# Kernel tuning notes

Hardware: AMD Instinct MI355X
Metric: run time of the kernel (lower is better)

Reference implementation:

```python
import jax, jax.numpy as jnp
import numpy as np

N_HEADS = 16
EMBED = 1024
HEAD_SIZE = 64
BLOCK = 2048
BATCH = 4


def setup_inputs() -> dict:
    key = jax.random.key(0)
    ks = jax.random.split(key, 6)
    s = 1.0 / np.sqrt(EMBED)
    X = jax.random.normal(ks[0], (BATCH, BLOCK, EMBED), dtype=jnp.float32)
    Wq = jax.random.normal(ks[1], (N_HEADS, EMBED, HEAD_SIZE), dtype=jnp.float32) * s
    Wk = jax.random.normal(ks[2], (N_HEADS, EMBED, HEAD_SIZE), dtype=jnp.float32) * s
    Wv = jax.random.normal(ks[3], (N_HEADS, EMBED, HEAD_SIZE), dtype=jnp.float32) * s
    Wo = jax.random.normal(ks[4], (EMBED, EMBED), dtype=jnp.float32) * s
    bo = jnp.zeros((EMBED,), dtype=jnp.float32)
    return {"X": X, "Wq": Wq, "Wk": Wk, "Wv": Wv, "Wo": Wo, "bo": bo}


def reference(X, Wq, Wk, Wv, Wo, bo):
    # X: [B, S, E]; Wq/Wk/Wv: [H, E, Dh]
    q = jnp.einsum("bse,hed->bhsd", X, Wq)
    k = jnp.einsum("bse,hed->bhsd", X, Wk)
    v = jnp.einsum("bse,hed->bhsd", X, Wv)
    scale = 1.0 / np.sqrt(HEAD_SIZE)
    scores = jnp.einsum("bhsd,bhtd->bhst", q, k) * scale  # [B,H,S,S]
    S = X.shape[1]
    causal = jnp.tril(jnp.ones((S, S), dtype=bool))
    scores = jnp.where(causal, scores, -jnp.inf)
    wei = jax.nn.softmax(scores, axis=-1)
    # dropout p=0.2 treated as identity (eval mode) for deterministic reference
    out = jnp.einsum("bhst,bhtd->bhsd", wei, v)  # [B,H,S,Dh]
    out = out.transpose(0, 2, 1, 3).reshape(X.shape[0], S, N_HEADS * HEAD_SIZE)
    return out @ Wo.T + bo
```

## Files before the change

### kernel.cpp

```cpp
#include <hip/hip_runtime.h>
#include <stdint.h>


typedef __bf16 bf16_t;
typedef __bf16 bf16x4 __attribute__((ext_vector_type(4)));
typedef __bf16 bf16x8 __attribute__((ext_vector_type(8)));
typedef float  f32x4  __attribute__((ext_vector_type(4)));
typedef float  f32x16 __attribute__((ext_vector_type(16)));
typedef unsigned int u32;

union V8 { bf16x8 v8; bf16x4 h[2]; u32 w[4]; };

__device__ __forceinline__ void gload_lds16(const void* g, void* l) {
  __builtin_amdgcn_global_load_lds((const __attribute__((address_space(1))) void*)g,
                                   (__attribute__((address_space(3))) void*)l, 16, 0, 0);
}


__global__ void mha_cvt_bf16(const float* __restrict__ in, bf16_t* __restrict__ out) {
  size_t i = ((size_t)blockIdx.x * 256 + threadIdx.x) * 8;
  const float4* p = (const float4*)(in + i);
  float4 a = p[0], b = p[1];
  bf16x8 o;
  o[0] = (__bf16)a.x; o[1] = (__bf16)a.y; o[2] = (__bf16)a.z; o[3] = (__bf16)a.w;
  o[4] = (__bf16)b.x; o[5] = (__bf16)b.y; o[6] = (__bf16)b.z; o[7] = (__bf16)b.w;
  *(bf16x8*)(out + i) = o;
}

__global__ void mha_prep_w(const float* __restrict__ Wq, const float* __restrict__ Wk,
                           const float* __restrict__ Wv, bf16_t* __restrict__ Wt) {
  __shared__ float tile[64][65];
  const int e0 = blockIdx.x * 64;
  const int mh = blockIdx.y;
  const int mat = mh >> 4, h = mh & 15;
  const float* W = (mat == 0) ? Wq : (mat == 1) ? Wk : Wv;
  #pragma unroll
  for (int i = 0; i < 16; i++) {
    int idx = threadIdx.x + i * 256;
    int er = idx >> 6, d = idx & 63;
    tile[er][d] = W[(size_t)(h * 1024 + e0 + er) * 64 + d];
  }
  __syncthreads();
  #pragma unroll
  for (int i = 0; i < 16; i++) {
    int idx = threadIdx.x + i * 256;
    int dr = idx >> 6, ec = idx & 63;
    Wt[(size_t)(mat * 1024 + h * 64 + dr) * 1024 + e0 + ec] = (bf16_t)tile[ec][dr];
  }
}


template <int MODE>
__global__ __launch_bounds__(256) void gemm_bt(const bf16_t* __restrict__ A,
                                               const bf16_t* __restrict__ Bt,
                                               void* __restrict__ Cout,
                                               const float* __restrict__ bias,
                                               int M, int N, int K) {
  __shared__ bf16_t lA[128 * 32];
  __shared__ bf16_t lB[128 * 32];
  const int tid = threadIdx.x;
  const int l = tid & 63, w = tid >> 6;
  const int g = l >> 4, lg = l & 15;
  const int wr = w >> 1, wc = w & 1;
  const long brow = (long)blockIdx.y * 128;
  const long bcol = (long)blockIdx.x * 128;

  f32x4 acc[4][4];
  #pragma unroll
  for (int m = 0; m < 4; m++)
    #pragma unroll
    for (int n = 0; n < 4; n++) acc[m][n] = (f32x4){0.f, 0.f, 0.f, 0.f};

  const bf16_t* Ab = A + brow * K;
  const bf16_t* Bb = Bt + bcol * K;
  const int c0 = tid, c1 = tid + 256;
  const int r0 = c0 >> 2, o0 = (c0 & 3) * 8;
  const int r1 = c1 >> 2, o1 = (c1 & 3) * 8;

  for (int k0 = 0; k0 < K; k0 += 32) {
    __syncthreads();
    gload_lds16(Ab + (long)r0 * K + k0 + o0, lA + c0 * 8);
    gload_lds16(Ab + (long)r1 * K + k0 + o1, lA + c1 * 8);
    gload_lds16(Bb + (long)r0 * K + k0 + o0, lB + c0 * 8);
    gload_lds16(Bb + (long)r1 * K + k0 + o1, lB + c1 * 8);
    __syncthreads();
    bf16x8 af[4], bfr[4];
    #pragma unroll
    for (int m = 0; m < 4; m++)
      af[m] = *(const bf16x8*)(lA + (wr * 64 + m * 16 + lg) * 32 + g * 8);
    #pragma unroll
    for (int n = 0; n < 4; n++)
      bfr[n] = *(const bf16x8*)(lB + (wc * 64 + n * 16 + lg) * 32 + g * 8);
    #pragma unroll
    for (int m = 0; m < 4; m++)
      #pragma unroll
      for (int n = 0; n < 4; n++)
        acc[m][n] = __builtin_amdgcn_mfma_f32_16x16x32_bf16(af[m], bfr[n], acc[m][n], 0, 0, 0);
  }

  #pragma unroll
  for (int m = 0; m < 4; m++) {
    #pragma unroll
    for (int n = 0; n < 4; n++) {
      long row0 = brow + wr * 64 + m * 16 + g * 4;
      long col  = bcol + wc * 64 + n * 16 + lg;
      if (MODE == 0) {
        bf16_t* C = (bf16_t*)Cout;
        #pragma unroll
        for (int r = 0; r < 4; r++) C[(row0 + r) * N + col] = (bf16_t)acc[m][n][r];
      } else {
        float* C = (float*)Cout;
        float bv = bias[col];
        #pragma unroll
        for (int r = 0; r < 4; r++) C[(row0 + r) * N + col] = acc[m][n][r] + bv;
      }
    }
  }
}


__global__ __launch_bounds__(256, 4) void mha_attn3(const bf16_t* __restrict__ QKV,
                                                    bf16_t* __restrict__ AO) {
  __shared__ __align__(16) char smem[32768];
  const int tid = threadIdx.x;
  const int l = tid & 63, w = tid >> 6;
  const int q31 = l & 31;
  const int hi = l >> 5;
  const int hb = (l >> 4) & 1;
  const int lg = l & 15;

  const int bid = blockIdx.x;
  const int xcd = bid & 7, ii = bid >> 3;
  const int bh = xcd * 8 + (ii & 7);
  const int stripe = 15 - (ii >> 3);
  const int b = bh >> 4, h = bh & 15;

  const int qw = stripe * 128 + w * 32;
  const bf16_t* Qp = QKV + (size_t)b * 2048 * 3072 + h * 64;
  const bf16_t* Kp = Qp + 1024;
  const bf16_t* Vp = Qp + 2048;

  bf16x8 qf[4];
  {
    const bf16_t* qrow = Qp + (size_t)(qw + q31) * 3072 + hi * 8;
    #pragma unroll
    for (int ks = 0; ks < 4; ks++) qf[ks] = *(const bf16x8*)(qrow + ks * 16);
  }

  f32x16 o0, o1;
  #pragma unroll
  for (int r = 0; r < 16; r++) { o0[r] = 0.f; o1[r] = 0.f; }
  float m = -1e30f, lsum = 0.f;
  const float Cf = 0.18033688011112042f;

  const int tmaxw = 2 * stripe + 1 + (w >> 1);
  const int T = 2 * stripe + 2;
  const u32 ldsbase = (u32)(uintptr_t)(__attribute__((address_space(3))) char*)smem;

  auto stage = [&](int tt, int bi) {
    char* kb = smem + bi * 8192;
    char* vb = smem + 16384 + bi * 8192;
    #pragma unroll
    for (int it = 0; it < 2; it++) {
      int c = tid + it * 256;
      int row = c >> 3, cb = (c & 7) * 16;
      int scb = cb ^ ((row & 7) << 4);
      gload_lds16(Kp + (size_t)(tt * 64 + row) * 3072 + (scb >> 1), kb + c * 16);
      int st = c >> 5, qq = c & 31;
      int j = (st >> 2) * 16 + (qq >> 1), d = (st & 3) * 16 + (qq & 1) * 8;
      gload_lds16(Vp + (size_t)(tt * 64 + j) * 3072 + d, vb + c * 16);
    }
  };

  stage(0, 0);
  for (int t = 0; t < T; t++) {
    const int cur = t & 1;
    if (t + 1 < T) {
      stage(t + 1, cur ^ 1);
      __builtin_amdgcn_sched_barrier(0);
      asm volatile("s_waitcnt vmcnt(4)" ::: "memory");
    } else {
      __builtin_amdgcn_sched_barrier(0);
      asm volatile("s_waitcnt vmcnt(0)" ::: "memory");
    }
    __builtin_amdgcn_sched_barrier(0);
    __builtin_amdgcn_s_barrier();
    __builtin_amdgcn_sched_barrier(0);

    const bool active = (t < tmaxw);
    u32 paw[4][4];
    if (active) {
      f32x16 p0, p1;
      #pragma unroll
      for (int r = 0; r < 16; r++) { p0[r] = 0.f; p1[r] = 0.f; }
      {
        const char* kb = smem + cur * 8192;
        const int rb0 = q31 * 128;
        const int swz = (l & 7) << 4;
        __builtin_amdgcn_s_setprio(1);
        #pragma unroll
        for (int ks = 0; ks < 4; ks++) {
          int colb = ((ks << 5) | (hi << 4)) ^ swz;
          bf16x8 kf0 = *(const bf16x8*)(kb + rb0 + colb);
          bf16x8 kf1 = *(const bf16x8*)(kb + 4096 + rb0 + colb);
          p0 = __builtin_amdgcn_mfma_f32_32x32x16_bf16(kf0, qf[ks], p0, 0, 0, 0);
          p1 = __builtin_amdgcn_mfma_f32_32x32x16_bf16(kf1, qf[ks], p1, 0, 0, 0);
        }
        __builtin_amdgcn_s_setprio(0);
      }
      if (t == tmaxw - 1) {
        int q = qw + q31;
        int kvb = t * 64 + 4 * hi;
        #pragma unroll
        for (int r = 0; r < 16; r++) {
          int kv0 = kvb + (r & 3) + 8 * (r >> 2);
          if (kv0 > q) p0[r] = -1e30f;
          if (kv0 + 32 > q) p1[r] = -1e30f;
        }
      }
      float t8[8];
      #pragma unroll
      for (int r = 0; r < 8; r++)
        t8[r] = fmaxf(fmaxf(p0[r], p0[r + 8]), fmaxf(p1[r], p1[r + 8]));
      float pm = fmaxf(fmaxf(fmaxf(t8[0], t8[4]), fmaxf(t8[1], t8[5])),
                       fmaxf(fmaxf(t8[2], t8[6]), fmaxf(t8[3], t8[7])));
      pm = fmaxf(pm, __shfl_xor(pm, 32));
      if (!__all(pm - m <= 64.f)) {
        float mn = fmaxf(m, pm);
        float alpha = exp2f((m - mn) * Cf);
        #pragma unroll
        for (int r = 0; r < 16; r++) { o0[r] *= alpha; o1[r] *= alpha; }
        lsum *= alpha;
        m = mn;
      }
      float mc = m * Cf;
      #pragma unroll
      for (int r = 0; r < 16; r++) p0[r] = exp2f(fmaf(p0[r], Cf, -mc));
      #pragma unroll
      for (int r = 0; r < 16; r++) p1[r] = exp2f(fmaf(p1[r], Cf, -mc));
      float s8[8];
      #pragma unroll
      for (int r = 0; r < 8; r++)
        s8[r] = (p0[r] + p0[r + 8]) + (p1[r] + p1[r + 8]);
      float rs = ((s8[0] + s8[1]) + (s8[2] + s8[3])) + ((s8[4] + s8[5]) + (s8[6] + s8[7]));
      rs += __shfl_xor(rs, 32);
      lsum += rs;
      #pragma unroll
      for (int gblk = 0; gblk < 4; gblk++) {
        int base = (gblk & 1) * 8;
        float e0 = (gblk < 2) ? p0[base + 0] : p1[base + 0];
        float e1 = (gblk < 2) ? p0[base + 1] : p1[base + 1];
        float e2 = (gblk < 2) ? p0[base + 2] : p1[base + 2];
        float e3 = (gblk < 2) ? p0[base + 3] : p1[base + 3];
        float e4 = (gblk < 2) ? p0[base + 4] : p1[base + 4];
        float e5 = (gblk < 2) ? p0[base + 5] : p1[base + 5];
        float e6 = (gblk < 2) ? p0[base + 6] : p1[base + 6];
        float e7 = (gblk < 2) ? p0[base + 7] : p1[base + 7];
        u32 u0, u1, v0, v1;
        asm("v_cvt_pk_bf16_f32 %0, %1, %2" : "=v"(u0) : "v"(e0), "v"(e1));
        asm("v_cvt_pk_bf16_f32 %0, %1, %2" : "=v"(u1) : "v"(e2), "v"(e3));
        asm("v_cvt_pk_bf16_f32 %0, %1, %2" : "=v"(v0) : "v"(e4), "v"(e5));
        asm("v_cvt_pk_bf16_f32 %0, %1, %2" : "=v"(v1) : "v"(e6), "v"(e7));
        asm("v_permlane32_swap_b32 %0, %1" : "+v"(u0), "+v"(v0));
        asm("v_permlane32_swap_b32 %0, %1" : "+v"(u1), "+v"(v1));
        paw[gblk][0] = u0; paw[gblk][1] = u1; paw[gblk][2] = v0; paw[gblk][3] = v1;
      }
      V8 vf[2][4];
      u32 vb = ldsbase + 16384u + (u32)cur * 8192u;
      #pragma unroll
      for (int mb = 0; mb < 2; mb++)
        #pragma unroll
        for (int ks = 0; ks < 4; ks++) {
          u32 base = vb + (u32)(((ks * 4 + 2 * mb + hb) << 9) + hi * 256 + lg * 8);
          bf16x4 t0, t1;
          asm volatile("ds_read_b64_tr_b16 %0, %1" : "=v"(t0) : "v"(base));
          asm volatile("ds_read_b64_tr_b16 %0, %1 offset:128" : "=v"(t1) : "v"(base));
          vf[mb][ks].h[0] = t0; vf[mb][ks].h[1] = t1;
        }
      asm volatile("s_waitcnt lgkmcnt(0)" ::: "memory");
      __builtin_amdgcn_sched_barrier(0);
      __builtin_amdgcn_s_setprio(1);
      #pragma unroll
      for (int ks = 0; ks < 4; ks++) {
        V8 pa; pa.w[0] = paw[ks][0]; pa.w[1] = paw[ks][1]; pa.w[2] = paw[ks][2]; pa.w[3] = paw[ks][3];
        o0 = __builtin_amdgcn_mfma_f32_32x32x16_bf16(vf[0][ks].v8, pa.v8, o0, 0, 0, 0);
        o1 = __builtin_amdgcn_mfma_f32_32x32x16_bf16(vf[1][ks].v8, pa.v8, o1, 0, 0, 0);
      }
      __builtin_amdgcn_s_setprio(0);
    }
    __builtin_amdgcn_sched_barrier(0);
    __builtin_amdgcn_s_barrier();
    __builtin_amdgcn_sched_barrier(0);
  }

  float linv = 1.f / lsum;
  __syncthreads();
  bf16_t* ow = (bf16_t*)smem + w * 2048;
  #pragma unroll
  for (int mb = 0; mb < 2; mb++)
    #pragma unroll
    for (int r = 0; r < 16; r += 2) {
      int d = mb * 32 + (r & 3) + 8 * (r >> 2) + 4 * hi;
      float a0 = (mb ? o1[r] : o0[r]) * linv;
      float a1 = (mb ? o1[r + 1] : o0[r + 1]) * linv;
      u32 pk;
      asm("v_cvt_pk_bf16_f32 %0, %1, %2" : "=v"(pk) : "v"(a0), "v"(a1));
      int byteoff = q31 * 128 + ((d * 2) ^ ((q31 & 7) << 4));
      *(u32*)((char*)ow + byteoff) = pk;
    }
  __syncthreads();
  const size_t aorow0 = (size_t)b * 2048 + qw;
  #pragma unroll
  for (int it = 0; it < 4; it++) {
    int idx = it * 64 + l;
    int q = idx >> 3, c = idx & 7;
    bf16x8 v8 = *(const bf16x8*)((const char*)ow + q * 128 + ((c * 16) ^ ((q & 7) << 4)));
    *(bf16x8*)(AO + (aorow0 + q) * 1024 + h * 64 + c * 8) = v8;
  }
}


extern "C" void kernel_launch(void* const* d_in, const int* in_sizes, int n_in,
                              void* d_out, int out_size, void* d_ws, size_t ws_size,
                              hipStream_t stream) {
  (void)in_sizes; (void)n_in; (void)out_size; (void)ws_size;
  const float* X  = (const float*)d_in[0];
  const float* Wq = (const float*)d_in[1];
  const float* Wk = (const float*)d_in[2];
  const float* Wv = (const float*)d_in[3];
  const float* Wo = (const float*)d_in[4];
  const float* bo = (const float*)d_in[5];
  float* out = (float*)d_out;

  char* ws = (char*)d_ws;
  bf16_t* Xb  = (bf16_t*)ws;
  bf16_t* AO  = Xb;
  bf16_t* Wt  = (bf16_t*)(ws + (16u << 20));
  bf16_t* Wob = (bf16_t*)(ws + (22u << 20));
  bf16_t* QKV = (bf16_t*)(ws + (24u << 20));

  mha_cvt_bf16<<<dim3(4096), dim3(256), 0, stream>>>(X, Xb);
  mha_prep_w<<<dim3(16, 48), dim3(256), 0, stream>>>(Wq, Wk, Wv, Wt);
  mha_cvt_bf16<<<dim3(512), dim3(256), 0, stream>>>(Wo, Wob);
  gemm_bt<0><<<dim3(3072 / 128, 8192 / 128), dim3(256), 0, stream>>>(
      Xb, Wt, (void*)QKV, nullptr, 8192, 3072, 1024);
  mha_attn3<<<dim3(1024), dim3(256), 0, stream>>>(QKV, AO);
  gemm_bt<1><<<dim3(1024 / 128, 8192 / 128), dim3(256), 0, stream>>>(
      AO, Wob, (void*)out, bo, 8192, 1024, 1024);
}
```

Measured before the change: 188.5 us.

## Pair long and short causal stripes per workgroup for balanced attention work

Each attention workgroup now handles two query stripes, a high one (15-pair) and a low one (pair), so every workgroup does the same total number of KV tiles and the causal load imbalance goes away. The grid is halved to 512 workgroups, and the K/V prefetch pipeline carries across from the first stripe into the second. The first stripe's accumulators stay in registers until both epilogues run, which raises register pressure, so launch bounds drop to 2 waves per SIMD. Fewer workgroups means less parallelism to hide latency.

```diff
diff --git a/kernel.cpp b/kernel.cpp
--- a/kernel.cpp
+++ b/kernel.cpp
@@ -119,7 +119,7 @@
 }
 
 
-__global__ __launch_bounds__(256, 4) void mha_attn3(const bf16_t* __restrict__ QKV,
+__global__ __launch_bounds__(256, 2) void mha_attn4(const bf16_t* __restrict__ QKV,
                                                     bf16_t* __restrict__ AO) {
   __shared__ __align__(16) char smem[32768];
   const int tid = threadIdx.x;
@@ -130,34 +130,31 @@
   const int lg = l & 15;
 
   const int bid = blockIdx.x;
-  const int xcd = bid & 7, ii = bid >> 3;
-  const int bh = xcd * 8 + (ii & 7);
-  const int stripe = 15 - (ii >> 3);
+  const int wgid = (bid & 7) * 64 + (bid >> 3);
+  const int bh = wgid >> 3, pair = wgid & 7;
   const int b = bh >> 4, h = bh & 15;
-
-  const int qw = stripe * 128 + w * 32;
+  const int s_hi = 15 - pair, s_lo = pair;
+  const int T_hi = 2 * s_hi + 2;
+
   const bf16_t* Qp = QKV + (size_t)b * 2048 * 3072 + h * 64;
   const bf16_t* Kp = Qp + 1024;
   const bf16_t* Vp = Qp + 2048;
 
-  bf16x8 qf[4];
+  bf16x8 qfh[4], qfl[4];
   {
-    const bf16_t* qrow = Qp + (size_t)(qw + q31) * 3072 + hi * 8;
-    #pragma unroll
-    for (int ks = 0; ks < 4; ks++) qf[ks] = *(const bf16x8*)(qrow + ks * 16);
-  }
-
-  f32x16 o0, o1;
-  #pragma unroll
-  for (int r = 0; r < 16; r++) { o0[r] = 0.f; o1[r] = 0.f; }
-  float m = -1e30f, lsum = 0.f;
+    const bf16_t* qr0 = Qp + (size_t)(s_hi * 128 + w * 32 + q31) * 3072 + hi * 8;
+    const bf16_t* qr1 = Qp + (size_t)(s_lo * 128 + w * 32 + q31) * 3072 + hi * 8;
+    #pragma unroll
+    for (int ks = 0; ks < 4; ks++) {
+      qfh[ks] = *(const bf16x8*)(qr0 + ks * 16);
+      qfl[ks] = *(const bf16x8*)(qr1 + ks * 16);
+    }
+  }
+
   const float Cf = 0.18033688011112042f;
-
-  const int tmaxw = 2 * stripe + 1 + (w >> 1);
-  const int T = 2 * stripe + 2;
   const u32 ldsbase = (u32)(uintptr_t)(__attribute__((address_space(3))) char*)smem;
 
-  auto stage = [&](int tt, int bi) {
+  auto stage = [&](int kt, int bi) {
     char* kb = smem + bi * 8192;
     char* vb = smem + 16384 + bi * 8192;
     #pragma unroll
@@ -165,157 +162,184 @@
       int c = tid + it * 256;
       int row = c >> 3, cb = (c & 7) * 16;
       int scb = cb ^ ((row & 7) << 4);
-      gload_lds16(Kp + (size_t)(tt * 64 + row) * 3072 + (scb >> 1), kb + c * 16);
+      gload_lds16(Kp + (size_t)(kt * 64 + row) * 3072 + (scb >> 1), kb + c * 16);
       int st = c >> 5, qq = c & 31;
       int j = (st >> 2) * 16 + (qq >> 1), d = (st & 3) * 16 + (qq & 1) * 8;
-      gload_lds16(Vp + (size_t)(tt * 64 + j) * 3072 + d, vb + c * 16);
+      gload_lds16(Vp + (size_t)(kt * 64 + j) * 3072 + d, vb + c * 16);
     }
   };
 
+  auto epilogue = [&](const f32x16& e0, const f32x16& e1, float ls, int qw) {
+    float linv = 1.f / ls;
+    __syncthreads();
+    bf16_t* ow = (bf16_t*)smem + w * 2048;
+    #pragma unroll
+    for (int mb = 0; mb < 2; mb++)
+      #pragma unroll
+      for (int r = 0; r < 16; r += 2) {
+        int d = mb * 32 + (r & 3) + 8 * (r >> 2) + 4 * hi;
+        float a0 = (mb ? e1[r] : e0[r]) * linv;
+        float a1 = (mb ? e1[r + 1] : e0[r + 1]) * linv;
+        u32 pk;
+        asm("v_cvt_pk_bf16_f32 %0, %1, %2" : "=v"(pk) : "v"(a0), "v"(a1));
+        int byteoff = q31 * 128 + ((d * 2) ^ ((q31 & 7) << 4));
+        *(u32*)((char*)ow + byteoff) = pk;
+      }
+    __syncthreads();
+    const size_t aorow0 = (size_t)b * 2048 + qw;
+    #pragma unroll
+    for (int it = 0; it < 4; it++) {
+      int idx = it * 64 + l;
+      int q = idx >> 3, c = idx & 7;
+      bf16x8 v8 = *(const bf16x8*)((const char*)ow + q * 128 + ((c * 16) ^ ((q & 7) << 4)));
+      *(bf16x8*)(AO + (aorow0 + q) * 1024 + h * 64 + c * 8) = v8;
+    }
+  };
+
+  f32x16 oh0, oh1;
+  float lsum_h = 0.f;
+
   stage(0, 0);
-  for (int t = 0; t < T; t++) {
-    const int cur = t & 1;
-    if (t + 1 < T) {
-      stage(t + 1, cur ^ 1);
+  #pragma unroll
+  for (int st = 0; st < 2; st++) {
+    const int s = st == 0 ? s_hi : s_lo;
+    const int qw = s * 128 + w * 32;
+    const int T = 2 * s + 2;
+    const int tmaxw = 2 * s + 1 + (w >> 1);
+
+    f32x16 o0, o1;
+    #pragma unroll
+    for (int r = 0; r < 16; r++) { o0[r] = 0.f; o1[r] = 0.f; }
+    float m = -1e30f, lsum = 0.f;
+
+    for (int t = 0; t < T; t++) {
+      const int cur = t & 1;
+      const bool last_global = (st == 1) && (t + 1 == T);
+      if (!last_global) {
+        int nk = (st == 0) ? ((t + 1 < T) ? t + 1 : 0) : t + 1;
+        stage(nk, cur ^ 1);
+        __builtin_amdgcn_sched_barrier(0);
+        asm volatile("s_waitcnt vmcnt(4)" ::: "memory");
+      } else {
+        __builtin_amdgcn_sched_barrier(0);
+        asm volatile("s_waitcnt vmcnt(0)" ::: "memory");
+      }
       __builtin_amdgcn_sched_barrier(0);
-      asm volatile("s_waitcnt vmcnt(4)" ::: "memory");
-    } else {
+      __builtin_amdgcn_s_barrier();
       __builtin_amdgcn_sched_barrier(0);
-      asm volatile("s_waitcnt vmcnt(0)" ::: "memory");
-    }
-    __builtin_amdgcn_sched_barrier(0);
-    __builtin_amdgcn_s_barrier();
-    __builtin_amdgcn_sched_barrier(0);
-
-    const bool active = (t < tmaxw);
-    u32 paw[4][4];
-    if (active) {
-      f32x16 p0, p1;
-      #pragma unroll
-      for (int r = 0; r < 16; r++) { p0[r] = 0.f; p1[r] = 0.f; }
-      {
-        const char* kb = smem + cur * 8192;
-        const int rb0 = q31 * 128;
-        const int swz = (l & 7) << 4;
+
+      const bool active = (t < tmaxw);
+      u32 paw[4][4];
+      if (active) {
+        f32x16 p0, p1;
+        #pragma unroll
+        for (int r = 0; r < 16; r++) { p0[r] = 0.f; p1[r] = 0.f; }
+        {
+          const char* kb = smem + cur * 8192;
+          const int rb0 = q31 * 128;
+          const int swz = (l & 7) << 4;
+          __builtin_amdgcn_s_setprio(1);
+          #pragma unroll
+          for (int ks = 0; ks < 4; ks++) {
+            int colb = ((ks << 5) | (hi << 4)) ^ swz;
+            bf16x8 kf0 = *(const bf16x8*)(kb + rb0 + colb);
+            bf16x8 kf1 = *(const bf16x8*)(kb + 4096 + rb0 + colb);
+            bf16x8 qv = st == 0 ? qfh[ks] : qfl[ks];
+            p0 = __builtin_amdgcn_mfma_f32_32x32x16_bf16(kf0, qv, p0, 0, 0, 0);
+            p1 = __builtin_amdgcn_mfma_f32_32x32x16_bf16(kf1, qv, p1, 0, 0, 0);
+          }
+          __builtin_amdgcn_s_setprio(0);
+        }
+        if (t == tmaxw - 1) {
+          int q = qw + q31;
+          int kvb = t * 64 + 4 * hi;
+          #pragma unroll
+          for (int r = 0; r < 16; r++) {
+            int kv0 = kvb + (r & 3) + 8 * (r >> 2);
+            if (kv0 > q) p0[r] = -1e30f;
+            if (kv0 + 32 > q) p1[r] = -1e30f;
+          }
+        }
+        float t8[8];
+        #pragma unroll
+        for (int r = 0; r < 8; r++)
+          t8[r] = fmaxf(fmaxf(p0[r], p0[r + 8]), fmaxf(p1[r], p1[r + 8]));
+        float pm = fmaxf(fmaxf(fmaxf(t8[0], t8[4]), fmaxf(t8[1], t8[5])),
+                         fmaxf(fmaxf(t8[2], t8[6]), fmaxf(t8[3], t8[7])));
+        pm = fmaxf(pm, __shfl_xor(pm, 32));
+        if (!__all(pm - m <= 64.f)) {
+          float mn = fmaxf(m, pm);
+          float alpha = exp2f((m - mn) * Cf);
+          #pragma unroll
+          for (int r = 0; r < 16; r++) { o0[r] *= alpha; o1[r] *= alpha; }
+          lsum *= alpha;
+          m = mn;
+        }
+        float mc = m * Cf;
+        #pragma unroll
+        for (int r = 0; r < 16; r++) p0[r] = exp2f(fmaf(p0[r], Cf, -mc));
+        #pragma unroll
+        for (int r = 0; r < 16; r++) p1[r] = exp2f(fmaf(p1[r], Cf, -mc));
+        float s8[8];
+        #pragma unroll
+        for (int r = 0; r < 8; r++)
+          s8[r] = (p0[r] + p0[r + 8]) + (p1[r] + p1[r + 8]);
+        float rs = ((s8[0] + s8[1]) + (s8[2] + s8[3])) + ((s8[4] + s8[5]) + (s8[6] + s8[7]));
+        rs += __shfl_xor(rs, 32);
+        lsum += rs;
+        #pragma unroll
+        for (int gblk = 0; gblk < 4; gblk++) {
+          int base = (gblk & 1) * 8;
+          float e0 = (gblk < 2) ? p0[base + 0] : p1[base + 0];
+          float e1 = (gblk < 2) ? p0[base + 1] : p1[base + 1];
+          float e2 = (gblk < 2) ? p0[base + 2] : p1[base + 2];
+          float e3 = (gblk < 2) ? p0[base + 3] : p1[base + 3];
+          float e4 = (gblk < 2) ? p0[base + 4] : p1[base + 4];
+          float e5 = (gblk < 2) ? p0[base + 5] : p1[base + 5];
+          float e6 = (gblk < 2) ? p0[base + 6] : p1[base + 6];
+          float e7 = (gblk < 2) ? p0[base + 7] : p1[base + 7];
+          u32 u0, u1, v0, v1;
+          asm("v_cvt_pk_bf16_f32 %0, %1, %2" : "=v"(u0) : "v"(e0), "v"(e1));
+          asm("v_cvt_pk_bf16_f32 %0, %1, %2" : "=v"(u1) : "v"(e2), "v"(e3));
+          asm("v_cvt_pk_bf16_f32 %0, %1, %2" : "=v"(v0) : "v"(e4), "v"(e5));
+          asm("v_cvt_pk_bf16_f32 %0, %1, %2" : "=v"(v1) : "v"(e6), "v"(e7));
+          asm("v_permlane32_swap_b32 %0, %1" : "+v"(u0), "+v"(v0));
+          asm("v_permlane32_swap_b32 %0, %1" : "+v"(u1), "+v"(v1));
+          paw[gblk][0] = u0; paw[gblk][1] = u1; paw[gblk][2] = v0; paw[gblk][3] = v1;
+        }
+        V8 vf[2][4];
+        u32 vb = ldsbase + 16384u + (u32)cur * 8192u;
+        #pragma unroll
+        for (int mb = 0; mb < 2; mb++)
+          #pragma unroll
+          for (int ks = 0; ks < 4; ks++) {
+            u32 base = vb + (u32)(((ks * 4 + 2 * mb + hb) << 9) + hi * 256 + lg * 8);
+            bf16x4 t0, t1;
+            asm volatile("ds_read_b64_tr_b16 %0, %1" : "=v"(t0) : "v"(base));
+            asm volatile("ds_read_b64_tr_b16 %0, %1 offset:128" : "=v"(t1) : "v"(base));
+            vf[mb][ks].h[0] = t0; vf[mb][ks].h[1] = t1;
+          }
+        asm volatile("s_waitcnt lgkmcnt(0)" ::: "memory");
+        __builtin_amdgcn_sched_barrier(0);
         __builtin_amdgcn_s_setprio(1);
         #pragma unroll
         for (int ks = 0; ks < 4; ks++) {
-          int colb = ((ks << 5) | (hi << 4)) ^ swz;
-          bf16x8 kf0 = *(const bf16x8*)(kb + rb0 + colb);
-          bf16x8 kf1 = *(const bf16x8*)(kb + 4096 + rb0 + colb);
-          p0 = __builtin_amdgcn_mfma_f32_32x32x16_bf16(kf0, qf[ks], p0, 0, 0, 0);
-          p1 = __builtin_amdgcn_mfma_f32_32x32x16_bf16(kf1, qf[ks], p1, 0, 0, 0);
+          V8 pa; pa.w[0] = paw[ks][0]; pa.w[1] = paw[ks][1]; pa.w[2] = paw[ks][2]; pa.w[3] = paw[ks][3];
+          o0 = __builtin_amdgcn_mfma_f32_32x32x16_bf16(vf[0][ks].v8, pa.v8, o0, 0, 0, 0);
+          o1 = __builtin_amdgcn_mfma_f32_32x32x16_bf16(vf[1][ks].v8, pa.v8, o1, 0, 0, 0);
         }
         __builtin_amdgcn_s_setprio(0);
       }
-      if (t == tmaxw - 1) {
-        int q = qw + q31;
-        int kvb = t * 64 + 4 * hi;
-        #pragma unroll
-        for (int r = 0; r < 16; r++) {
-          int kv0 = kvb + (r & 3) + 8 * (r >> 2);
-          if (kv0 > q) p0[r] = -1e30f;
-          if (kv0 + 32 > q) p1[r] = -1e30f;
-        }
-      }
-      float t8[8];
-      #pragma unroll
-      for (int r = 0; r < 8; r++)
-        t8[r] = fmaxf(fmaxf(p0[r], p0[r + 8]), fmaxf(p1[r], p1[r + 8]));
-      float pm = fmaxf(fmaxf(fmaxf(t8[0], t8[4]), fmaxf(t8[1], t8[5])),
-                       fmaxf(fmaxf(t8[2], t8[6]), fmaxf(t8[3], t8[7])));
-      pm = fmaxf(pm, __shfl_xor(pm, 32));
-      if (!__all(pm - m <= 64.f)) {
-        float mn = fmaxf(m, pm);
-        float alpha = exp2f((m - mn) * Cf);
-        #pragma unroll
-        for (int r = 0; r < 16; r++) { o0[r] *= alpha; o1[r] *= alpha; }
-        lsum *= alpha;
-        m = mn;
-      }
-      float mc = m * Cf;
-      #pragma unroll
-      for (int r = 0; r < 16; r++) p0[r] = exp2f(fmaf(p0[r], Cf, -mc));
-      #pragma unroll
-      for (int r = 0; r < 16; r++) p1[r] = exp2f(fmaf(p1[r], Cf, -mc));
-      float s8[8];
-      #pragma unroll
-      for (int r = 0; r < 8; r++)
-        s8[r] = (p0[r] + p0[r + 8]) + (p1[r] + p1[r + 8]);
-      float rs = ((s8[0] + s8[1]) + (s8[2] + s8[3])) + ((s8[4] + s8[5]) + (s8[6] + s8[7]));
-      rs += __shfl_xor(rs, 32);
-      lsum += rs;
-      #pragma unroll
-      for (int gblk = 0; gblk < 4; gblk++) {
-        int base = (gblk & 1) * 8;
-        float e0 = (gblk < 2) ? p0[base + 0] : p1[base + 0];
-        float e1 = (gblk < 2) ? p0[base + 1] : p1[base + 1];
-        float e2 = (gblk < 2) ? p0[base + 2] : p1[base + 2];
-        float e3 = (gblk < 2) ? p0[base + 3] : p1[base + 3];
-        float e4 = (gblk < 2) ? p0[base + 4] : p1[base + 4];
-        float e5 = (gblk < 2) ? p0[base + 5] : p1[base + 5];
-        float e6 = (gblk < 2) ? p0[base + 6] : p1[base + 6];
-        float e7 = (gblk < 2) ? p0[base + 7] : p1[base + 7];
-        u32 u0, u1, v0, v1;
-        asm("v_cvt_pk_bf16_f32 %0, %1, %2" : "=v"(u0) : "v"(e0), "v"(e1));
-        asm("v_cvt_pk_bf16_f32 %0, %1, %2" : "=v"(u1) : "v"(e2), "v"(e3));
-        asm("v_cvt_pk_bf16_f32 %0, %1, %2" : "=v"(v0) : "v"(e4), "v"(e5));
-        asm("v_cvt_pk_bf16_f32 %0, %1, %2" : "=v"(v1) : "v"(e6), "v"(e7));
-        asm("v_permlane32_swap_b32 %0, %1" : "+v"(u0), "+v"(v0));
-        asm("v_permlane32_swap_b32 %0, %1" : "+v"(u1), "+v"(v1));
-        paw[gblk][0] = u0; paw[gblk][1] = u1; paw[gblk][2] = v0; paw[gblk][3] = v1;
-      }
-      V8 vf[2][4];
-      u32 vb = ldsbase + 16384u + (u32)cur * 8192u;
-      #pragma unroll
-      for (int mb = 0; mb < 2; mb++)
-        #pragma unroll
-        for (int ks = 0; ks < 4; ks++) {
-          u32 base = vb + (u32)(((ks * 4 + 2 * mb + hb) << 9) + hi * 256 + lg * 8);
-          bf16x4 t0, t1;
-          asm volatile("ds_read_b64_tr_b16 %0, %1" : "=v"(t0) : "v"(base));
-          asm volatile("ds_read_b64_tr_b16 %0, %1 offset:128" : "=v"(t1) : "v"(base));
-          vf[mb][ks].h[0] = t0; vf[mb][ks].h[1] = t1;
-        }
-      asm volatile("s_waitcnt lgkmcnt(0)" ::: "memory");
       __builtin_amdgcn_sched_barrier(0);
-      __builtin_amdgcn_s_setprio(1);
-      #pragma unroll
-      for (int ks = 0; ks < 4; ks++) {
-        V8 pa; pa.w[0] = paw[ks][0]; pa.w[1] = paw[ks][1]; pa.w[2] = paw[ks][2]; pa.w[3] = paw[ks][3];
-        o0 = __builtin_amdgcn_mfma_f32_32x32x16_bf16(vf[0][ks].v8, pa.v8, o0, 0, 0, 0);
-        o1 = __builtin_amdgcn_mfma_f32_32x32x16_bf16(vf[1][ks].v8, pa.v8, o1, 0, 0, 0);
-      }
-      __builtin_amdgcn_s_setprio(0);
-    }
-    __builtin_amdgcn_sched_barrier(0);
-    __builtin_amdgcn_s_barrier();
-    __builtin_amdgcn_sched_barrier(0);
-  }
-
-  float linv = 1.f / lsum;
-  __syncthreads();
-  bf16_t* ow = (bf16_t*)smem + w * 2048;
-  #pragma unroll
-  for (int mb = 0; mb < 2; mb++)
-    #pragma unroll
-    for (int r = 0; r < 16; r += 2) {
-      int d = mb * 32 + (r & 3) + 8 * (r >> 2) + 4 * hi;
-      float a0 = (mb ? o1[r] : o0[r]) * linv;
-      float a1 = (mb ? o1[r + 1] : o0[r + 1]) * linv;
-      u32 pk;
-      asm("v_cvt_pk_bf16_f32 %0, %1, %2" : "=v"(pk) : "v"(a0), "v"(a1));
-      int byteoff = q31 * 128 + ((d * 2) ^ ((q31 & 7) << 4));
-      *(u32*)((char*)ow + byteoff) = pk;
-    }
-  __syncthreads();
-  const size_t aorow0 = (size_t)b * 2048 + qw;
-  #pragma unroll
-  for (int it = 0; it < 4; it++) {
-    int idx = it * 64 + l;
-    int q = idx >> 3, c = idx & 7;
-    bf16x8 v8 = *(const bf16x8*)((const char*)ow + q * 128 + ((c * 16) ^ ((q & 7) << 4)));
-    *(bf16x8*)(AO + (aorow0 + q) * 1024 + h * 64 + c * 8) = v8;
+      __builtin_amdgcn_s_barrier();
+      __builtin_amdgcn_sched_barrier(0);
+    }
+
+    if (st == 0) { oh0 = o0; oh1 = o1; lsum_h = lsum; }
+    else {
+      epilogue(oh0, oh1, lsum_h, s_hi * 128 + w * 32);
+      epilogue(o0, o1, lsum, qw);
+    }
   }
 }
 
@@ -344,7 +368,7 @@
   mha_cvt_bf16<<<dim3(512), dim3(256), 0, stream>>>(Wo, Wob);
   gemm_bt<0><<<dim3(3072 / 128, 8192 / 128), dim3(256), 0, stream>>>(
       Xb, Wt, (void*)QKV, nullptr, 8192, 3072, 1024);
-  mha_attn3<<<dim3(1024), dim3(256), 0, stream>>>(QKV, AO);
+  mha_attn4<<<dim3(512), dim3(256), 0, stream>>>(QKV, AO);
   gemm_bt<1><<<dim3(1024 / 128, 8192 / 128), dim3(256), 0, stream>>>(
       AO, Wob, (void*)out, bo, 8192, 1024, 1024);
 }
```

Result: slower. 192.9 us (+2.3%).

## Add 256x256 pipelined QKV GEMM and rebalance causal attention block order

Applied to the files above, without the earlier changes.

Replaces the 128x128 QKV projection GEMM with a 512-thread 256x256 tile kernel. It uses 128KB of LDS holding a three-slot ring of K chunks, staged with direct global-to-LDS loads, and spreads the loads across eight compute phases with s_setprio around the MFMA bursts. Block IDs are swizzled across XCDs for reuse. The attention kernel's block-to-stripe mapping is also changed, pairing short and long causal stripes so per-wave work is more even. This trades occupancy (one large block per CU) for more data reuse per block and overlap of loads with compute.

```diff
diff --git a/kernel.cpp b/kernel.cpp
--- a/kernel.cpp
+++ b/kernel.cpp
@@ -47,6 +47,115 @@
     int dr = idx >> 6, ec = idx & 63;
     Wt[(size_t)(mat * 1024 + h * 64 + dr) * 1024 + e0 + ec] = (bf16_t)tile[ec][dr];
   }
+}
+
+
+__global__ __launch_bounds__(512, 2) void gemm256(const bf16_t* __restrict__ A,
+                                                  const bf16_t* __restrict__ Bt,
+                                                  bf16_t* __restrict__ C,
+                                                  int M, int N, int K) {
+  __shared__ __align__(16) char lds[131072];
+  const int tid = threadIdx.x;
+  const int l = tid & 63, w = tid >> 6;
+  const int g = l >> 4, lg = l & 15;
+  const int wr = w >> 2, wc = w & 3;
+  const int bid = blockIdx.x;
+  const int nbn = N >> 8;
+  const int gsw = (bid & 7) * (gridDim.x >> 3) + (bid >> 3);
+  const long brow = (long)(gsw / nbn) * 256;
+  const long bcol = (long)(gsw % nbn) * 256;
+
+  f32x4 acc[8][4];
+  #pragma unroll
+  for (int im = 0; im < 8; im++)
+    #pragma unroll
+    for (int n = 0; n < 4; n++) acc[im][n] = (f32x4){0.f, 0.f, 0.f, 0.f};
+
+  auto stage = [&](const bf16_t* base, long trow, int k0, int region) {
+    #pragma unroll
+    for (int j = 0; j < 2; j++) {
+      int p = (tid + j * 512) * 16;
+      gload_lds16(base + (trow + (p >> 6)) * (long)K + k0 + ((p & 63) >> 1),
+                  lds + region + p);
+    }
+  };
+
+  stage(A,  brow, 0,  0);
+  stage(Bt, bcol, 0,  65536);
+  stage(A,  brow, 32, 16384);
+  stage(Bt, bcol, 32, 65536 + 16384);
+  stage(A,  brow, 64, 32768);
+  stage(Bt, bcol, 64, 65536 + 32768);
+  asm volatile("s_waitcnt vmcnt(4)" ::: "memory");
+  __builtin_amdgcn_s_barrier();
+  __builtin_amdgcn_sched_barrier(0);
+
+  const int nIter = K >> 7;
+  for (int t = 0; t < nIter; t++) {
+    const bool more = (t + 1 < nIter);
+    const int kb = t * 128;
+    #pragma unroll
+    for (int ph = 0; ph < 8; ph++) {
+      const int slot = ph >> 2;
+      const int kh = (ph >> 1) & 1, mq = ph & 1;
+      bf16x8 af[4], bfv[4];
+      {
+        const char* pA = lds + slot * 32768 + kh * 16384;
+        const char* pB = pA + 65536;
+        #pragma unroll
+        for (int m = 0; m < 4; m++) {
+          int wrow = wr * 128 + mq * 64 + m * 16 + lg;
+          af[m] = *(const bf16x8*)(pA + wrow * 64 + g * 16);
+        }
+        #pragma unroll
+        for (int n = 0; n < 4; n++) {
+          int wrow = wc * 64 + n * 16 + lg;
+          bfv[n] = *(const bf16x8*)(pB + wrow * 64 + g * 16);
+        }
+      }
+      if (ph == 0)      stage(A,  brow, kb + 96,  32768 + 16384);
+      else if (ph == 1) stage(Bt, bcol, kb + 96,  65536 + 32768 + 16384);
+      else if (more) {
+        if (ph == 2)      stage(A,  brow, kb + 128, 0);
+        else if (ph == 3) stage(Bt, bcol, kb + 128, 65536);
+        else if (ph == 4) stage(A,  brow, kb + 160, 16384);
+        else if (ph == 5) stage(Bt, bcol, kb + 160, 65536 + 16384);
+        else if (ph == 6) stage(A,  brow, kb + 192, 32768);
+        else              stage(Bt, bcol, kb + 192, 65536 + 32768);
+      }
+      __builtin_amdgcn_s_barrier();
+      asm volatile("s_waitcnt lgkmcnt(0)" ::: "memory");
+      __builtin_amdgcn_sched_barrier(0);
+      __builtin_amdgcn_s_setprio(1);
+      #pragma unroll
+      for (int m = 0; m < 4; m++)
+        #pragma unroll
+        for (int n = 0; n < 4; n++)
+          acc[mq * 4 + m][n] =
+              __builtin_amdgcn_mfma_f32_16x16x32_bf16(af[m], bfv[n], acc[mq * 4 + m][n], 0, 0, 0);
+      __builtin_amdgcn_s_setprio(0);
+      __builtin_amdgcn_sched_barrier(0);
+      if (ph == 3) {
+        if (more) asm volatile("s_waitcnt vmcnt(4)" ::: "memory");
+        else      asm volatile("s_waitcnt vmcnt(0)" ::: "memory");
+      } else if (ph == 7 && more) {
+        asm volatile("s_waitcnt vmcnt(4)" ::: "memory");
+      }
+      __builtin_amdgcn_s_barrier();
+      __builtin_amdgcn_sched_barrier(0);
+    }
+  }
+
+  #pragma unroll
+  for (int im = 0; im < 8; im++)
+    #pragma unroll
+    for (int n = 0; n < 4; n++) {
+      long row0 = brow + wr * 128 + im * 16 + g * 4;
+      long col  = bcol + wc * 64 + n * 16 + lg;
+      #pragma unroll
+      for (int r = 0; r < 4; r++)
+        C[(row0 + r) * N + col] = (bf16_t)acc[im][n][r];
+    }
 }
 
 
@@ -105,14 +214,14 @@
       long row0 = brow + wr * 64 + m * 16 + g * 4;
       long col  = bcol + wc * 64 + n * 16 + lg;
       if (MODE == 0) {
-        bf16_t* C = (bf16_t*)Cout;
-        #pragma unroll
-        for (int r = 0; r < 4; r++) C[(row0 + r) * N + col] = (bf16_t)acc[m][n][r];
+        bf16_t* Cb = (bf16_t*)Cout;
+        #pragma unroll
+        for (int r = 0; r < 4; r++) Cb[(row0 + r) * N + col] = (bf16_t)acc[m][n][r];
       } else {
-        float* C = (float*)Cout;
+        float* Cf = (float*)Cout;
         float bv = bias[col];
         #pragma unroll
-        for (int r = 0; r < 4; r++) C[(row0 + r) * N + col] = acc[m][n][r] + bv;
+        for (int r = 0; r < 4; r++) Cf[(row0 + r) * N + col] = acc[m][n][r] + bv;
       }
     }
   }
@@ -130,9 +239,10 @@
   const int lg = l & 15;
 
   const int bid = blockIdx.x;
-  const int xcd = bid & 7, ii = bid >> 3;
-  const int bh = xcd * 8 + (ii & 7);
-  const int stripe = 15 - (ii >> 3);
+  const int c = bid & 255, k4 = bid >> 8;
+  const int s0 = c >> 6;
+  const int stripe = (k4 == 0) ? s0 : (k4 == 1) ? 15 - s0 : (k4 == 2) ? 7 - s0 : 8 + s0;
+  const int bh = c & 63;
   const int b = bh >> 4, h = bh & 15;
 
   const int qw = stripe * 128 + w * 32;
@@ -162,13 +272,13 @@
     char* vb = smem + 16384 + bi * 8192;
     #pragma unroll
     for (int it = 0; it < 2; it++) {
-      int c = tid + it * 256;
-      int row = c >> 3, cb = (c & 7) * 16;
+      int cc = tid + it * 256;
+      int row = cc >> 3, cb = (cc & 7) * 16;
       int scb = cb ^ ((row & 7) << 4);
-      gload_lds16(Kp + (size_t)(tt * 64 + row) * 3072 + (scb >> 1), kb + c * 16);
-      int st = c >> 5, qq = c & 31;
+      gload_lds16(Kp + (size_t)(tt * 64 + row) * 3072 + (scb >> 1), kb + cc * 16);
+      int st = cc >> 5, qq = cc & 31;
       int j = (st >> 2) * 16 + (qq >> 1), d = (st & 3) * 16 + (qq & 1) * 8;
-      gload_lds16(Vp + (size_t)(tt * 64 + j) * 3072 + d, vb + c * 16);
+      gload_lds16(Vp + (size_t)(tt * 64 + j) * 3072 + d, vb + cc * 16);
     }
   };
 
@@ -313,9 +423,9 @@
   #pragma unroll
   for (int it = 0; it < 4; it++) {
     int idx = it * 64 + l;
-    int q = idx >> 3, c = idx & 7;
-    bf16x8 v8 = *(const bf16x8*)((const char*)ow + q * 128 + ((c * 16) ^ ((q & 7) << 4)));
-    *(bf16x8*)(AO + (aorow0 + q) * 1024 + h * 64 + c * 8) = v8;
+    int q = idx >> 3, cc = idx & 7;
+    bf16x8 v8 = *(const bf16x8*)((const char*)ow + q * 128 + ((cc * 16) ^ ((q & 7) << 4)));
+    *(bf16x8*)(AO + (aorow0 + q) * 1024 + h * 64 + cc * 8) = v8;
   }
 }
 
@@ -342,8 +452,7 @@
   mha_cvt_bf16<<<dim3(4096), dim3(256), 0, stream>>>(X, Xb);
   mha_prep_w<<<dim3(16, 48), dim3(256), 0, stream>>>(Wq, Wk, Wv, Wt);
   mha_cvt_bf16<<<dim3(512), dim3(256), 0, stream>>>(Wo, Wob);
-  gemm_bt<0><<<dim3(3072 / 128, 8192 / 128), dim3(256), 0, stream>>>(
-      Xb, Wt, (void*)QKV, nullptr, 8192, 3072, 1024);
+  gemm256<<<dim3(384), dim3(512), 0, stream>>>(Xb, Wt, QKV, 8192, 3072, 1024);
   mha_attn3<<<dim3(1024), dim3(256), 0, stream>>>(QKV, AO);
   gemm_bt<1><<<dim3(1024 / 128, 8192 / 128), dim3(256), 0, stream>>>(
       AO, Wob, (void*)out, bo, 8192, 1024, 1024);
```

Result: no change. 192.0 us (+1.9%).
